# Kernel tuning notes

Hardware: AMD Instinct MI355X
Metric: run time of the kernel (lower is better)

The kernel has to match this reference:

```python
import jax, jax.numpy as jnp
import numpy as np

N, E, C = 4096, 32768, 64
IN, H, HEADS, L = 128, 256, 4, 2
HD = H // HEADS


def setup_inputs() -> dict:
    key = jax.random.key(0)
    ks = iter(jax.random.split(key, 40))
    s = lambda *sh: jax.random.normal(next(ks), sh, jnp.float32) * 0.05
    inp = {
        "node_features": jax.random.normal(next(ks), (N, IN), jnp.float32),
        "edges": jax.random.randint(next(ks), (E, 2), 0, N),
        "candidates": jax.random.randint(next(ks), (C, 2), 0, N),
        # GRUCell(input_dim, hidden_dim): torch layout w_ih [3H, IN], w_hh [3H, H]
        "gru_w_ih": s(3 * H, IN), "gru_w_hh": s(3 * H, H),
        "gru_b_ih": s(3 * H), "gru_b_hh": s(3 * H),
        # GraphTransformer: L layers of MHA + LN + FFN, stacked over layer dim
        "attn_in_w": s(L, 3 * H, H), "attn_in_b": s(L, 3 * H),
        "attn_out_w": s(L, H, H), "attn_out_b": s(L, H),
        "ln1_g": jnp.ones((L, H), jnp.float32), "ln1_b": jnp.zeros((L, H), jnp.float32),
        "ffn_w1": s(L, 4 * H, H), "ffn_b1": s(L, 4 * H),
        "ffn_w2": s(L, H, 4 * H), "ffn_b2": s(L, H),
        "ln2_g": jnp.ones((L, H), jnp.float32), "ln2_b": jnp.zeros((L, H), jnp.float32),
        # SCN
        "scn_w1": s(H, H), "scn_b1": s(H), "scn_w2": s(H, H), "scn_b2": s(H),
        # EdgePredictor: Linear(2H, H) -> ReLU -> Linear(H, 1)
        "ep_w1": s(H, 2 * H), "ep_b1": s(H), "ep_w2": s(1, H), "ep_b2": s(1),
    }
    return inp


def _layernorm(x, g, b, eps=1e-5):
    m = jnp.mean(x, -1, keepdims=True)
    v = jnp.mean((x - m) ** 2, -1, keepdims=True)
    return g * (x - m) / jnp.sqrt(v + eps) + b


def _mha(x, in_w, in_b, out_w, out_b):
    # x: [N, H]; torch MultiheadAttention self-attention, batch=1
    qkv = x @ in_w.T + in_b                      # [N, 3H]
    q, k, v = jnp.split(qkv, 3, axis=-1)
    q = q.reshape(N, HEADS, HD).transpose(1, 0, 2)  # [heads, N, hd]
    k = k.reshape(N, HEADS, HD).transpose(1, 0, 2)
    v = v.reshape(N, HEADS, HD).transpose(1, 0, 2)
    scores = jnp.einsum('hqd,hkd->hqk', q, k) / jnp.sqrt(jnp.float32(HD))
    a = jax.nn.softmax(scores, axis=-1)
    o = jnp.einsum('hqk,hkd->hqd', a, v).transpose(1, 0, 2).reshape(N, H)
    return o @ out_w.T + out_b


def _run_memory(node_features, edges, gru_w_ih, gru_w_hh, gru_b_ih, gru_b_hh):
    # input-gate contribution depends only on src feature: vectorize upfront
    gi_all = node_features[edges[:, 0]] @ gru_w_ih.T + gru_b_ih  # [E, 3H]

    def step(mem, inp):
        gi, dst = inp
        h = mem[dst]                                   # gather [H]
        gh = h @ gru_w_hh.T + gru_b_hh                 # [3H]
        ir, iz, inn = jnp.split(gi, 3)
        hr, hz, hn = jnp.split(gh, 3)
        r = jax.nn.sigmoid(ir + hr)
        z = jax.nn.sigmoid(iz + hz)
        n = jnp.tanh(inn + r * hn)
        h_new = (1.0 - z) * n + z * h                  # torch GRUCell update
        return mem.at[dst].set(h_new), None

    mem0 = jnp.zeros((N, H), jnp.float32)
    mem, _ = jax.lax.scan(step, mem0, (gi_all, edges[:, 1]))
    return mem


def reference(node_features, edges, candidates, gru_w_ih, gru_w_hh, gru_b_ih, gru_b_hh,
              attn_in_w, attn_in_b, attn_out_w, attn_out_b, ln1_g, ln1_b,
              ffn_w1, ffn_b1, ffn_w2, ffn_b2, ln2_g, ln2_b,
              scn_w1, scn_b1, scn_w2, scn_b2, ep_w1, ep_b1, ep_w2, ep_b2):
    mem = _run_memory(node_features, edges, gru_w_ih, gru_w_hh, gru_b_ih, gru_b_hh)
    x = jax.lax.stop_gradient(mem)   # original writes memory with .detach()
    for l in range(L):
        a = _mha(x, attn_in_w[l], attn_in_b[l], attn_out_w[l], attn_out_b[l])
        x = _layernorm(x + a, ln1_g[l], ln1_b[l])
        f = jax.nn.relu(x @ ffn_w1[l].T + ffn_b1[l]) @ ffn_w2[l].T + ffn_b2[l]
        x = _layernorm(x + f, ln2_g[l], ln2_b[l])
    refined = jax.nn.relu(x @ scn_w1.T + scn_b1) @ scn_w2.T + scn_b2
    h = jnp.concatenate([refined[candidates[:, 0]], refined[candidates[:, 1]]], axis=-1)  # [C, 2H]
    logits = jax.nn.relu(h @ ep_w1.T + ep_b1) @ ep_w2.T + ep_b2  # [C, 1]
    return jax.nn.sigmoid(logits).squeeze(-1)
```

## Files before the change

### kernel.cpp

```cpp
#include <hip/hip_runtime.h>
#include <math.h>

#define NN     4096
#define NE     32768
#define NCAND  64
#define IND    128
#define HDM    256
#define NL     2
#define MAXD   64
#define GNPB   16
#define NS     4

typedef __attribute__((ext_vector_type(8))) short short8;
typedef __attribute__((ext_vector_type(4))) float f32x4;

__device__ __forceinline__ float sigf(float x) { return 1.0f / (1.0f + __expf(-x)); }
__device__ __forceinline__ float tanh_fast(float x) {
  float e = __expf(-2.0f * fabsf(x));
  float r = (1.0f - e) / (1.0f + e);
  return x < 0.0f ? -r : r;
}
__device__ __forceinline__ unsigned short f2bf(float f) {
  unsigned int x = __float_as_uint(f);
  x += 0x7fffu + ((x >> 16) & 1u);
  return (unsigned short)(x >> 16);
}
__device__ __forceinline__ float bf2f(unsigned short u) {
  return __uint_as_float(((unsigned int)u) << 16);
}

#define CVT_TOT 2523136
__global__ __launch_bounds__(256) void cvt_weights(
    const float* __restrict__ nf, const float* __restrict__ wih,
    const float* __restrict__ ain, const float* __restrict__ aout,
    const float* __restrict__ f1, const float* __restrict__ f2,
    const float* __restrict__ s1, const float* __restrict__ s2,
    const float* __restrict__ whh, unsigned short* __restrict__ dst) {
  const size_t e = ((size_t)blockIdx.x * 256 + threadIdx.x) * 4;
  if (e >= CVT_TOT) return;
  const float* src;
  if (e < 524288)       src = nf   + e;
  else if (e < 622592)  src = wih  + (e - 524288);
  else if (e < 1015808) src = ain  + (e - 622592);
  else if (e < 1146880) src = aout + (e - 1015808);
  else if (e < 1671168) src = f1   + (e - 1146880);
  else if (e < 2195456) src = f2   + (e - 1671168);
  else if (e < 2260992) src = s1   + (e - 2195456);
  else if (e < 2326528) src = s2   + (e - 2260992);
  else                  src = whh  + (e - 2326528);
  const float4 v = *(const float4*)src;
  dst[e + 0] = f2bf(v.x); dst[e + 1] = f2bf(v.y);
  dst[e + 2] = f2bf(v.z); dst[e + 3] = f2bf(v.w);
}

__global__ __launch_bounds__(256) void build_pos(const int* __restrict__ edges,
                                                 int* __restrict__ cnt, int* __restrict__ lists) {
  const int e = blockIdx.x * 256 + threadIdx.x;
  const int d = edges[2 * e + 1];
  const int slot = atomicAdd(&cnt[d], 1);
  if (slot < MAXD) lists[(size_t)d * MAXD + slot] = e;
}

__global__ __launch_bounds__(256) void sort_srcs(const int* __restrict__ edges,
                                                 int* __restrict__ cnt,
                                                 const int* __restrict__ lists,
                                                 int* __restrict__ srcs,
                                                 int* __restrict__ hist) {
  __shared__ int Ls[256][65];
  const int t = threadIdx.x;
  const int d = blockIdx.x * 256 + t;
  int c = cnt[d]; if (c > MAXD) c = MAXD;
  for (int i = 0; i < c; ++i) Ls[t][i] = lists[(size_t)d * MAXD + i];
  for (int i = 1; i < c; ++i) {
    const int key = Ls[t][i];
    int j = i - 1;
    while (j >= 0 && Ls[t][j] > key) { Ls[t][j + 1] = Ls[t][j]; --j; }
    Ls[t][j + 1] = key;
  }
  for (int i = 0; i < c; ++i) srcs[(size_t)d * MAXD + i] = edges[2 * Ls[t][i]];
  cnt[d] = c;
  atomicAdd(&hist[c], 1);
}

__global__ void scan_prep(const int* __restrict__ hist, int* __restrict__ cursor) {
  const int t = threadIdx.x;
  if (t <= MAXD) {
    int ss = 0;
    for (int dd = t + 1; dd <= MAXD; ++dd) ss += hist[dd];
    cursor[t] = ss;
  }
}

__global__ __launch_bounds__(256) void perm_scatter(const int* __restrict__ cnt,
                                                    int* __restrict__ cursor, int* __restrict__ perm) {
  const int d = blockIdx.x * 256 + threadIdx.x;
  const int rank = atomicAdd(&cursor[cnt[d]], 1);
  perm[rank] = d;
}

__global__ void prep_bias(const float* __restrict__ b_ih, const float* __restrict__ b_hh,
                          float* __restrict__ bias_gx) {
  const int t = blockIdx.x * 256 + threadIdx.x;
  if (t < 768) bias_gx[t] = b_ih[t] + (t < 512 ? b_hh[t] : 0.0f);
}

template <int ACT, int GS, int OMODE>
__global__ __launch_bounds__(256) void gemm_bf16(
    const unsigned short* __restrict__ A, const int* __restrict__ gidx,
    const unsigned short* __restrict__ W, const float* __restrict__ bias,
    float* __restrict__ C, unsigned short* __restrict__ Cb,
    int M, int N, int K) {
  __shared__ unsigned short As[64 * 64];
  __shared__ unsigned short Ws[64 * 64];
  __shared__ int ridx[64];
  const int bm = blockIdx.y * 64, bn = blockIdx.x * 64;
  const int tid = threadIdx.x;
  const int ln = tid & 63, w = tid >> 6;
  const int jc = ln & 15, kq = ln >> 4;
  const int srow = tid >> 2, q = tid & 3;

  if constexpr (GS > 0) {
    if (tid < 64) ridx[tid] = gidx[(size_t)(bm + tid) * GS];
    __syncthreads();
  }
  const size_t arow = (GS > 0) ? (size_t)ridx[srow] : (size_t)(bm + srow);
  const unsigned short* Asrc = A + arow * K + q * 16;
  const unsigned short* Wsrc = W + (size_t)(bn + srow) * K + q * 16;

  f32x4 acc[2][2];
#pragma unroll
  for (int i = 0; i < 2; ++i)
#pragma unroll
    for (int j = 0; j < 2; ++j) acc[i][j] = (f32x4){0.f, 0.f, 0.f, 0.f};
  const int mrow = (w >> 1) * 32, ncol = (w & 1) * 32;
  const int sb0 = (q * 32) ^ ((srow & 7) << 4);
  const int sb1 = (q * 32 + 16) ^ ((srow & 7) << 4);

  for (int k0 = 0; k0 < K; k0 += 64) {
    __syncthreads();
    {
      const short8 a0 = *(const short8*)(Asrc + k0);
      const short8 a1 = *(const short8*)(Asrc + k0 + 8);
      const short8 w0 = *(const short8*)(Wsrc + k0);
      const short8 w1 = *(const short8*)(Wsrc + k0 + 8);
      *(short8*)((char*)As + srow * 128 + sb0) = a0;
      *(short8*)((char*)As + srow * 128 + sb1) = a1;
      *(short8*)((char*)Ws + srow * 128 + sb0) = w0;
      *(short8*)((char*)Ws + srow * 128 + sb1) = w1;
    }
    __syncthreads();
#pragma unroll
    for (int kt = 0; kt < 2; ++kt) {
      const int kb = kt * 64 + kq * 16;
      short8 a[2], bb[2];
#pragma unroll
      for (int i = 0; i < 2; ++i) {
        const int ra = mrow + i * 16 + jc;
        a[i] = *(const short8*)((const char*)As + ra * 128 + (kb ^ ((ra & 7) << 4)));
        const int rb = ncol + i * 16 + jc;
        bb[i] = *(const short8*)((const char*)Ws + rb * 128 + (kb ^ ((rb & 7) << 4)));
      }
#pragma unroll
      for (int mi = 0; mi < 2; ++mi)
#pragma unroll
        for (int ni = 0; ni < 2; ++ni)
          acc[mi][ni] = __builtin_amdgcn_mfma_f32_16x16x32_bf16(a[mi], bb[ni], acc[mi][ni], 0, 0, 0);
    }
  }
#pragma unroll
  for (int mi = 0; mi < 2; ++mi)
#pragma unroll
    for (int ni = 0; ni < 2; ++ni) {
      const int col = bn + ncol + ni * 16 + jc;
      const float bs = bias[col];
#pragma unroll
      for (int v = 0; v < 4; ++v) {
        const int row = bm + mrow + mi * 16 + kq * 4 + v;
        float val = acc[mi][ni][v] + bs;
        if (ACT == 1) val = fmaxf(val, 0.0f);
        if constexpr (OMODE != 2) C[(size_t)row * N + col] = val;
        if constexpr (OMODE >= 1) Cb[(size_t)row * N + col] = f2bf(val);
      }
    }
}

__global__ __launch_bounds__(512, 1) void gru_reg(
    const int* __restrict__ perm, const int* __restrict__ cnt,
    const int* __restrict__ srcs, const unsigned short* __restrict__ gx,
    const unsigned short* __restrict__ whhb, const float* __restrict__ b_hh,
    float* __restrict__ x, unsigned short* __restrict__ xb) {
  const int tid = threadIdx.x;
  const int w = tid >> 6;
  const int ln = tid & 63;
  const int jc = ln & 15, kq = ln >> 4;
  const int grow = tid >> 5, gpart = tid & 31;

  __shared__ unsigned short Ah[GNPB * 256];
  __shared__ unsigned short Gi[GNPB * 776];
  __shared__ int srcs_s[GNPB][MAXD];
  __shared__ int node_s[GNPB], cnt_s[GNPB];
  __shared__ int Rb_s;

  if (tid < GNPB) {
    const int node = perm[blockIdx.x * GNPB + tid];
    node_s[tid] = node;
    cnt_s[tid] = cnt[node];
  }
  for (int i = tid; i < GNPB * 256; i += 512) Ah[i] = 0;
  __syncthreads();
  for (int i = tid; i < GNPB * MAXD; i += 512)
    srcs_s[i >> 6][i & 63] = srcs[(size_t)node_s[i >> 6] * MAXD + (i & 63)];
  if (tid == 0) {
    int mx = 0;
    for (int i = 0; i < GNPB; ++i) mx = mx > cnt_s[i] ? mx : cnt_s[i];
    Rb_s = mx;
  }

  short8 W[48];
#pragma unroll
  for (int g = 0; g < 3; ++g)
#pragma unroll
    for (int ct = 0; ct < 2; ++ct) {
      const unsigned short* src =
          whhb + (size_t)(g * 256 + w * 32 + ct * 16 + jc) * 256 + kq * 8;
#pragma unroll
      for (int kt = 0; kt < 8; ++kt)
        W[(g * 2 + ct) * 8 + kt] = *(const short8*)(src + kt * 32);
    }
  float bhN[2];
  bhN[0] = b_hh[512 + w * 32 + jc];
  bhN[1] = b_hh[512 + w * 32 + 16 + jc];

  float h[8];
#pragma unroll
  for (int i = 0; i < 8; ++i) h[i] = 0.f;

  __syncthreads();
  const int Rb = Rb_s;
  const int myc = cnt_s[grow];

  for (int r = 0; r < Rb; ++r) {
    const int sn = (r < myc) ? srcs_s[grow][r] : 0;
    const unsigned short* gsrc = gx + (size_t)sn * 768 + gpart * 24;
    const short8 gv0 = *(const short8*)gsrc;
    const short8 gv1 = *(const short8*)(gsrc + 8);
    const short8 gv2 = *(const short8*)(gsrc + 16);

    f32x4 acc[6];
#pragma unroll
    for (int i = 0; i < 6; ++i) acc[i] = (f32x4){0.f, 0.f, 0.f, 0.f};
#pragma unroll
    for (int kt = 0; kt < 8; ++kt) {
      const short8 a = *(const short8*)((const char*)Ah + jc * 512 +
                                        ((kt * 64 + kq * 16) ^ ((jc & 7) << 4)));
#pragma unroll
      for (int t = 0; t < 6; ++t)
        acc[t] = __builtin_amdgcn_mfma_f32_16x16x32_bf16(a, W[t * 8 + kt], acc[t], 0, 0, 0);
    }
    {
      unsigned short* gdst = Gi + grow * 776 + gpart * 24;
      *(short8*)gdst = gv0;
      *(short8*)(gdst + 8) = gv1;
      *(short8*)(gdst + 16) = gv2;
    }
    __syncthreads();
#pragma unroll
    for (int ct = 0; ct < 2; ++ct) {
      const int col = w * 32 + ct * 16 + jc;
#pragma unroll
      for (int v = 0; v < 4; ++v) {
        const int nd = kq * 4 + v;
        if (r < cnt_s[nd]) {
          const float giR = bf2f(Gi[nd * 776 + col]);
          const float giZ = bf2f(Gi[nd * 776 + 256 + col]);
          const float giN = bf2f(Gi[nd * 776 + 512 + col]);
          const float rr = sigf(giR + acc[ct][v]);
          const float zz = sigf(giZ + acc[2 + ct][v]);
          const float nn2 = tanh_fast(giN + rr * (acc[4 + ct][v] + bhN[ct]));
          const float hn = (1.0f - zz) * nn2 + zz * h[ct * 4 + v];
          h[ct * 4 + v] = hn;
          *(unsigned short*)((char*)Ah + nd * 512 + ((col * 2) ^ ((nd & 7) << 4))) = f2bf(hn);
        }
      }
    }
    __syncthreads();
  }
#pragma unroll
  for (int ct = 0; ct < 2; ++ct) {
    const int col = w * 32 + ct * 16 + jc;
#pragma unroll
    for (int v = 0; v < 4; ++v) {
      const int gnode = node_s[kq * 4 + v];
      x[(size_t)gnode * HDM + col] = h[ct * 4 + v];
      xb[(size_t)gnode * HDM + col] = f2bf(h[ct * 4 + v]);
    }
  }
}

__global__ __launch_bounds__(256) void transpose_v(const unsigned short* __restrict__ qkvb,
                                                   unsigned short* __restrict__ vtb) {
  const int h = blockIdx.y, nt = blockIdx.x;
  __shared__ unsigned short T[64][72];
  const int t = threadIdx.x;
  const int r = t >> 2, c = (t & 3) << 4;
  {
    const unsigned short* src = qkvb + (size_t)(nt * 64 + r) * 768 + 512 + h * 64 + c;
    *(short8*)&T[r][c] = *(const short8*)src;
    *(short8*)&T[r][c + 8] = *(const short8*)(src + 8);
  }
  __syncthreads();
  {
    short8 o0, o1;
#pragma unroll
    for (int j = 0; j < 8; ++j) { o0[j] = (short)T[c + j][r]; o1[j] = (short)T[c + 8 + j][r]; }
    unsigned short* dst = vtb + (size_t)(h * 64 + r) * 4096 + nt * 64 + c;
    *(short8*)dst = o0;
    *(short8*)(dst + 8) = o1;
  }
}

__global__ __launch_bounds__(256) void flash_part(
    const unsigned short* __restrict__ qkvb, const unsigned short* __restrict__ vtb,
    float* __restrict__ Op, float* __restrict__ lp) {
  const int h = blockIdx.y;
  const int qb = blockIdx.x * 64;
  const int z = blockIdx.z;
  const int tid = threadIdx.x;
  const int ln = tid & 63, w = tid >> 6;
  const int jc = ln & 15, kq = ln >> 4;
  __shared__ unsigned short Ks[2][64 * 64];
  __shared__ unsigned short Vts[2][64 * 64];
  __shared__ unsigned short Ps[4][16 * 64];

  short8 aq[2];
  {
    const unsigned short* qsrc = qkvb + (size_t)(qb + w * 16 + jc) * 768 + h * 64 + kq * 8;
    aq[0] = *(const short8*)qsrc;
    aq[1] = *(const short8*)(qsrc + 32);
  }
  f32x4 accO[4];
#pragma unroll
  for (int nf = 0; nf < 4; ++nf) accO[nf] = (f32x4){0.f, 0.f, 0.f, 0.f};
  float psum[4] = {0.f, 0.f, 0.f, 0.f};

  const int srow = tid >> 2, sc = tid & 3;
  const int swb0 = (sc * 32) ^ ((srow & 7) << 4);
  const int swb1 = (sc * 32 + 16) ^ ((srow & 7) << 4);
  const int k0 = z * 1024;
  unsigned short* Pw = Ps[w];

  short8 kr0, kr1, vr0, vr1;
  {
    const unsigned short* ksrc = qkvb + (size_t)(k0 + srow) * 768 + 256 + h * 64 + sc * 16;
    kr0 = *(const short8*)ksrc; kr1 = *(const short8*)(ksrc + 8);
    const unsigned short* vsrc = vtb + (size_t)(h * 64 + srow) * 4096 + k0 + sc * 16;
    vr0 = *(const short8*)vsrc; vr1 = *(const short8*)(vsrc + 8);
  }

  for (int t = 0; t < 16; ++t) {
    const int cur = t & 1;
    *(short8*)((char*)Ks[cur] + srow * 128 + swb0) = kr0;
    *(short8*)((char*)Ks[cur] + srow * 128 + swb1) = kr1;
    *(short8*)((char*)Vts[cur] + srow * 128 + swb0) = vr0;
    *(short8*)((char*)Vts[cur] + srow * 128 + swb1) = vr1;
    {
      const int tn = t < 15 ? t + 1 : 15;
      const unsigned short* ksrc =
          qkvb + (size_t)(k0 + tn * 64 + srow) * 768 + 256 + h * 64 + sc * 16;
      kr0 = *(const short8*)ksrc; kr1 = *(const short8*)(ksrc + 8);
      const unsigned short* vsrc =
          vtb + (size_t)(h * 64 + srow) * 4096 + k0 + tn * 64 + sc * 16;
      vr0 = *(const short8*)vsrc; vr1 = *(const short8*)(vsrc + 8);
    }
    __syncthreads();
    f32x4 s[4];
#pragma unroll
    for (int kt = 0; kt < 4; ++kt) s[kt] = (f32x4){0.f, 0.f, 0.f, 0.f};
    __builtin_amdgcn_s_setprio(1);
#pragma unroll
    for (int ks = 0; ks < 2; ++ks) {
#pragma unroll
      for (int kt = 0; kt < 4; ++kt) {
        const int brow = kt * 16 + jc;
        const short8 bk = *(const short8*)((const char*)Ks[cur] + brow * 128 +
                                           ((ks * 64 + kq * 16) ^ ((brow & 7) << 4)));
        s[kt] = __builtin_amdgcn_mfma_f32_16x16x32_bf16(aq[ks], bk, s[kt], 0, 0, 0);
      }
    }
    __builtin_amdgcn_s_setprio(0);
#pragma unroll
    for (int kt = 0; kt < 4; ++kt) {
#pragma unroll
      for (int v = 0; v < 4; ++v) {
        const float pv = __expf(s[kt][v] * 0.125f - 8.0f);
        psum[v] += pv;
        const int pr = kq * 4 + v;
        const int cb = kt * 32 + jc * 2;
        *(unsigned short*)((char*)Pw + pr * 128 + (cb ^ ((pr & 7) << 4))) = f2bf(pv);
      }
    }
    asm volatile("s_waitcnt lgkmcnt(0)" ::: "memory");
    __builtin_amdgcn_sched_barrier(0);
    __builtin_amdgcn_s_setprio(1);
#pragma unroll
    for (int ks = 0; ks < 2; ++ks) {
      const short8 ap = *(const short8*)((const char*)Pw + jc * 128 +
                                         ((ks * 64 + kq * 16) ^ ((jc & 7) << 4)));
#pragma unroll
      for (int nf = 0; nf < 4; ++nf) {
        const int brow = nf * 16 + jc;
        const short8 bv = *(const short8*)((const char*)Vts[cur] + brow * 128 +
                                           ((ks * 64 + kq * 16) ^ ((brow & 7) << 4)));
        accO[nf] = __builtin_amdgcn_mfma_f32_16x16x32_bf16(ap, bv, accO[nf], 0, 0, 0);
      }
    }
    __builtin_amdgcn_s_setprio(0);
  }
#pragma unroll
  for (int v = 0; v < 4; ++v) {
    float ps = psum[v];
    ps += __shfl_xor(ps, 1);
    ps += __shfl_xor(ps, 2);
    ps += __shfl_xor(ps, 4);
    ps += __shfl_xor(ps, 8);
    psum[v] = ps;
  }
  float* opb = Op + ((size_t)z * NN + qb + w * 16 + kq * 4) * HDM + h * 64 + jc;
#pragma unroll
  for (int nf = 0; nf < 4; ++nf)
#pragma unroll
    for (int v = 0; v < 4; ++v)
      opb[(size_t)v * HDM + nf * 16] = accO[nf][v];
  if (jc == 0) {
#pragma unroll
    for (int v = 0; v < 4; ++v)
      lp[((size_t)z * 4 + h) * NN + qb + w * 16 + kq * 4 + v] = psum[v];
  }
}

__global__ __launch_bounds__(256) void attn_combine(const float* __restrict__ Op,
                                                    const float* __restrict__ lp,
                                                    unsigned short* __restrict__ outb) {
  const int row = blockIdx.x * 4 + (threadIdx.x >> 6);
  const int lane = threadIdx.x & 63;
  const int col = lane * 4;
  const int h = col >> 6;
  float l = 0.f;
  float4 o = {0.f, 0.f, 0.f, 0.f};
#pragma unroll
  for (int z = 0; z < NS; ++z) {
    l += lp[((size_t)z * 4 + h) * NN + row];
    const float4 p = *(const float4*)(Op + ((size_t)z * NN + row) * HDM + col);
    o.x += p.x; o.y += p.y; o.z += p.z; o.w += p.w;
  }
  const float inv = 1.0f / l;
  unsigned short* d = outb + (size_t)row * HDM + col;
  d[0] = f2bf(o.x * inv); d[1] = f2bf(o.y * inv);
  d[2] = f2bf(o.z * inv); d[3] = f2bf(o.w * inv);
}

__global__ __launch_bounds__(256) void ln_residual(float* __restrict__ x,
                                                   const float* __restrict__ a,
                                                   const float* __restrict__ g,
                                                   const float* __restrict__ b,
                                                   unsigned short* __restrict__ xb) {
  const int lane = threadIdx.x & 63;
  const int row = blockIdx.x * 4 + (threadIdx.x >> 6);
  float v[4];
  float s = 0.0f;
#pragma unroll
  for (int j = 0; j < 4; j++) {
    const int col = j * 64 + lane;
    v[j] = x[(size_t)row * HDM + col] + a[(size_t)row * HDM + col];
    s += v[j];
  }
#pragma unroll
  for (int off = 32; off > 0; off >>= 1) s += __shfl_xor(s, off);
  const float mu = s * (1.0f / HDM);
  float vs = 0.0f;
#pragma unroll
  for (int j = 0; j < 4; j++) {
    const float d = v[j] - mu;
    vs += d * d;
  }
#pragma unroll
  for (int off = 32; off > 0; off >>= 1) vs += __shfl_xor(vs, off);
  const float rinv = 1.0f / sqrtf(vs * (1.0f / HDM) + 1e-5f);
#pragma unroll
  for (int j = 0; j < 4; j++) {
    const int col = j * 64 + lane;
    const float val = g[col] * (v[j] - mu) * rinv + b[col];
    x[(size_t)row * HDM + col] = val;
    xb[(size_t)row * HDM + col] = f2bf(val);
  }
}

template <int ACT>
__global__ __launch_bounds__(256) void gemm_bias(const float* __restrict__ A,
                                                 const float* __restrict__ W,
                                                 const float* __restrict__ bias,
                                                 float* __restrict__ C, int M, int NCo, int K) {
  __shared__ float As[16][65];
  __shared__ float Ws[16][65];
  const int bm = blockIdx.y * 64, bn = blockIdx.x * 64;
  const int tid = threadIdx.x;
  const int tx = tid & 15, ty = tid >> 4;
  const int lr = tid >> 2;
  const int lk = (tid & 3) * 4;
  float acc[4][4] = {{0.0f}};
  for (int k0 = 0; k0 < K; k0 += 16) {
    __syncthreads();
    {
      const float4 a4 = *(const float4*)(A + (size_t)(bm + lr) * K + k0 + lk);
      As[lk + 0][lr] = a4.x; As[lk + 1][lr] = a4.y; As[lk + 2][lr] = a4.z; As[lk + 3][lr] = a4.w;
      const float4 w4 = *(const float4*)(W + (size_t)(bn + lr) * K + k0 + lk);
      Ws[lk + 0][lr] = w4.x; Ws[lk + 1][lr] = w4.y; Ws[lk + 2][lr] = w4.z; Ws[lk + 3][lr] = w4.w;
    }
    __syncthreads();
#pragma unroll
    for (int k = 0; k < 16; k++) {
      const float a0 = As[k][ty * 4 + 0], a1 = As[k][ty * 4 + 1];
      const float a2 = As[k][ty * 4 + 2], a3 = As[k][ty * 4 + 3];
      const float w0 = Ws[k][tx * 4 + 0], w1 = Ws[k][tx * 4 + 1];
      const float w2 = Ws[k][tx * 4 + 2], w3 = Ws[k][tx * 4 + 3];
      acc[0][0] += a0 * w0; acc[0][1] += a0 * w1; acc[0][2] += a0 * w2; acc[0][3] += a0 * w3;
      acc[1][0] += a1 * w0; acc[1][1] += a1 * w1; acc[1][2] += a1 * w2; acc[1][3] += a1 * w3;
      acc[2][0] += a2 * w0; acc[2][1] += a2 * w1; acc[2][2] += a2 * w2; acc[2][3] += a2 * w3;
      acc[3][0] += a3 * w0; acc[3][1] += a3 * w1; acc[3][2] += a3 * w2; acc[3][3] += a3 * w3;
    }
  }
  const float b0 = bias[bn + tx * 4 + 0], b1 = bias[bn + tx * 4 + 1];
  const float b2 = bias[bn + tx * 4 + 2], b3 = bias[bn + tx * 4 + 3];
#pragma unroll
  for (int i = 0; i < 4; i++) {
    float4 o;
    o.x = acc[i][0] + b0; o.y = acc[i][1] + b1; o.z = acc[i][2] + b2; o.w = acc[i][3] + b3;
    if (ACT == 1) {
      o.x = fmaxf(o.x, 0.0f); o.y = fmaxf(o.y, 0.0f);
      o.z = fmaxf(o.z, 0.0f); o.w = fmaxf(o.w, 0.0f);
    }
    *(float4*)(C + (size_t)(bm + ty * 4 + i) * NCo + bn + tx * 4) = o;
  }
}

__global__ void gather_cat(const float* __restrict__ refined, const int* __restrict__ cand,
                           float* __restrict__ hcat) {
  const int c = blockIdx.x;
  const int t = threadIdx.x;
  const int n0 = cand[2 * c], n1 = cand[2 * c + 1];
  hcat[(size_t)c * 512 + t] = (t < 256) ? refined[(size_t)n0 * HDM + t]
                                        : refined[(size_t)n1 * HDM + (t - 256)];
}

__global__ void ep_final(const float* __restrict__ eph, const float* __restrict__ w2,
                         const float* __restrict__ b2, float* __restrict__ out) {
  const int c = blockIdx.x;
  const int lane = threadIdx.x;
  float s = 0.0f;
#pragma unroll
  for (int j = 0; j < 4; j++) s += eph[(size_t)c * HDM + j * 64 + lane] * w2[j * 64 + lane];
#pragma unroll
  for (int off = 32; off > 0; off >>= 1) s += __shfl_xor(s, off);
  if (lane == 0) out[c] = 1.0f / (1.0f + __expf(-(s + b2[0])));
}

extern "C" void kernel_launch(void* const* d_in, const int* in_sizes, int n_in,
                              void* d_out, int out_size, void* d_ws, size_t ws_size,
                              hipStream_t stream) {
  (void)in_sizes; (void)n_in; (void)out_size; (void)ws_size;
  const float* nf    = (const float*)d_in[0];
  const int*   edges = (const int*)d_in[1];
  const int*   cand  = (const int*)d_in[2];
  const float* w_ih  = (const float*)d_in[3];
  const float* w_hh  = (const float*)d_in[4];
  const float* b_ih  = (const float*)d_in[5];
  const float* b_hh  = (const float*)d_in[6];
  const float* ain_w = (const float*)d_in[7];
  const float* ain_b = (const float*)d_in[8];
  const float* aout_w = (const float*)d_in[9];
  const float* aout_b = (const float*)d_in[10];
  const float* ln1g = (const float*)d_in[11];
  const float* ln1b = (const float*)d_in[12];
  const float* f1w  = (const float*)d_in[13];
  const float* f1b  = (const float*)d_in[14];
  const float* f2w  = (const float*)d_in[15];
  const float* f2b  = (const float*)d_in[16];
  const float* ln2g = (const float*)d_in[17];
  const float* ln2b = (const float*)d_in[18];
  const float* s1w  = (const float*)d_in[19];
  const float* s1b  = (const float*)d_in[20];
  const float* s2w  = (const float*)d_in[21];
  const float* s2b  = (const float*)d_in[22];
  const float* e1w  = (const float*)d_in[23];
  const float* e1b  = (const float*)d_in[24];
  const float* e2w  = (const float*)d_in[25];
  const float* e2b  = (const float*)d_in[26];
  float* out = (float*)d_out;

  char* wp = (char*)d_ws;
  float* x        = (float*)wp; wp += (size_t)NN * HDM * 4;
  unsigned short* xb = (unsigned short*)wp; wp += (size_t)NN * HDM * 2;
  unsigned short* wseg = (unsigned short*)wp; wp += (size_t)CVT_TOT * 2;
  int* cnt        = (int*)wp;  wp += (size_t)NN * 4;
  int* lists      = (int*)wp;  wp += (size_t)NN * MAXD * 4;
  int* srcs       = (int*)wp;  wp += (size_t)NN * MAXD * 4;
  int* meta       = (int*)wp;  wp += 256 * 4;
  float* bias_gx  = (float*)wp; wp += 1024 * 4;
  int* perm       = (int*)wp;  wp += (size_t)NN * 4;
  unsigned short* gx = (unsigned short*)wp; wp += (size_t)NN * 768 * 2;
  char* uni       = wp;
  unsigned short* qkvb   = (unsigned short*)uni;
  unsigned short* vtb    = (unsigned short*)(uni + 6291456);
  float* abuf    = (float*)(uni + 8388608);
  unsigned short* abuf_b = (unsigned short*)(uni + 12582912);
  float* fbuf    = (float*)(uni + 14680064);
  float* Op      = fbuf;
  unsigned short* fbuf_b = (unsigned short*)(uni + 31457280);
  float* lp      = (float*)(uni + 31457280);
  float* refined = (float*)(uni + 39845888);
  float* hcat    = (float*)(uni + 44040192);
  float* eph     = (float*)(uni + 44171264);

  unsigned short* nf_b  = wseg;
  unsigned short* wihb  = wseg + 524288;
  unsigned short* ainb  = wseg + 622592;
  unsigned short* aoutb = wseg + 1015808;
  unsigned short* f1b_  = wseg + 1146880;
  unsigned short* f2b_  = wseg + 1671168;
  unsigned short* s1b_  = wseg + 2195456;
  unsigned short* s2b_  = wseg + 2260992;
  unsigned short* whhb  = wseg + 2326528;

  int* hist   = meta;
  int* cursor = meta + 128;

  hipMemsetAsync(cnt, 0, (size_t)NN * 4, stream);
  hipMemsetAsync(meta, 0, 256 * 4, stream);

  cvt_weights<<<2464, 256, 0, stream>>>(nf, w_ih, ain_w, aout_w, f1w, f2w, s1w, s2w, w_hh, wseg);
  build_pos<<<NE / 256, 256, 0, stream>>>(edges, cnt, lists);
  sort_srcs<<<NN / 256, 256, 0, stream>>>(edges, cnt, lists, srcs, hist);
  scan_prep<<<1, 128, 0, stream>>>(hist, cursor);
  perm_scatter<<<NN / 256, 256, 0, stream>>>(cnt, cursor, perm);
  prep_bias<<<3, 256, 0, stream>>>(b_ih, b_hh, bias_gx);

  gemm_bf16<0, 0, 2><<<dim3(12, NN / 64), 256, 0, stream>>>(
      nf_b, nullptr, wihb, bias_gx, nullptr, gx, NN, 768, IND);
  gru_reg<<<NN / GNPB, 512, 0, stream>>>(perm, cnt, srcs, gx, whhb, b_hh, x, xb);

  for (int l = 0; l < NL; l++) {
    gemm_bf16<0, 0, 2><<<dim3(12, 64), 256, 0, stream>>>(
        xb, nullptr, ainb + (size_t)l * 196608, ain_b + l * 768, nullptr, qkvb, NN, 768, HDM);
    transpose_v<<<dim3(64, 4), 256, 0, stream>>>(qkvb, vtb);
    flash_part<<<dim3(64, 4, NS), 256, 0, stream>>>(qkvb, vtb, Op, lp);
    attn_combine<<<NN / 4, 256, 0, stream>>>(Op, lp, abuf_b);
    gemm_bf16<0, 0, 0><<<dim3(4, 64), 256, 0, stream>>>(
        abuf_b, nullptr, aoutb + (size_t)l * 65536, aout_b + l * 256, fbuf, nullptr, NN, 256, HDM);
    ln_residual<<<NN / 4, 256, 0, stream>>>(x, fbuf, ln1g + l * 256, ln1b + l * 256, xb);
    gemm_bf16<1, 0, 2><<<dim3(16, 64), 256, 0, stream>>>(
        xb, nullptr, f1b_ + (size_t)l * 262144, f1b + l * 1024, nullptr, fbuf_b, NN, 1024, HDM);
    gemm_bf16<0, 0, 0><<<dim3(4, 64), 256, 0, stream>>>(
        fbuf_b, nullptr, f2b_ + (size_t)l * 262144, f2b + l * 256, abuf, nullptr, NN, 256, 1024);
    ln_residual<<<NN / 4, 256, 0, stream>>>(x, abuf, ln2g + l * 256, ln2b + l * 256, xb);
  }

  gemm_bf16<1, 0, 1><<<dim3(4, 64), 256, 0, stream>>>(
      xb, nullptr, s1b_, s1b, abuf, abuf_b, NN, 256, HDM);
  gemm_bf16<0, 0, 0><<<dim3(4, 64), 256, 0, stream>>>(
      abuf_b, nullptr, s2b_, s2b, refined, nullptr, NN, 256, HDM);
  gather_cat<<<NCAND, 512, 0, stream>>>(refined, cand, hcat);
  gemm_bias<1><<<dim3(4, 1), 256, 0, stream>>>(hcat, e1w, e1b, eph, NCAND, 256, 512);
  ep_final<<<NCAND, 64, 0, stream>>>(eph, e2w, e2b, out);
}
```

Baseline: 390.9 us.

## Fuse small kernels, write transposed V in QKV GEMM, prefetch GRU inputs

Merges the bias prep into the scan kernel and folds gather, edge-predictor GEMM and final sigmoid into one ep_fused kernel, cutting launch count. The QKV GEMM epilogue now also writes V transposed directly, so the separate transpose_v pass and its round trip through memory go away. The GRU recurrence loop software-prefetches the next step's gate inputs from global memory before the MFMA work to hide load latency. The transposed-V stores are narrow and strided, and the fused edge predictor reads fp32 weights per thread without tiling.

```diff
diff --git a/kernel.cpp b/kernel.cpp
--- a/kernel.cpp
+++ b/kernel.cpp
@@ -12,6 +12,7 @@
 #define NS     4
 
 typedef __attribute__((ext_vector_type(8))) short short8;
+typedef __attribute__((ext_vector_type(4))) short short4b;
 typedef __attribute__((ext_vector_type(4))) float f32x4;
 
 __device__ __forceinline__ float sigf(float x) { return 1.0f / (1.0f + __expf(-x)); }
@@ -82,12 +83,21 @@
   atomicAdd(&hist[c], 1);
 }
 
-__global__ void scan_prep(const int* __restrict__ hist, int* __restrict__ cursor) {
-  const int t = threadIdx.x;
-  if (t <= MAXD) {
-    int ss = 0;
-    for (int dd = t + 1; dd <= MAXD; ++dd) ss += hist[dd];
-    cursor[t] = ss;
+__global__ __launch_bounds__(256) void scan_prep(const int* __restrict__ hist,
+                                                 int* __restrict__ cursor,
+                                                 const float* __restrict__ b_ih,
+                                                 const float* __restrict__ b_hh,
+                                                 float* __restrict__ bias_gx) {
+  if (blockIdx.x == 3) {
+    const int t = threadIdx.x;
+    if (t <= MAXD) {
+      int ss = 0;
+      for (int dd = t + 1; dd <= MAXD; ++dd) ss += hist[dd];
+      cursor[t] = ss;
+    }
+  } else {
+    const int gt = blockIdx.x * 256 + threadIdx.x;
+    if (gt < 768) bias_gx[gt] = b_ih[gt] + (gt < 512 ? b_hh[gt] : 0.0f);
   }
 }
 
@@ -98,18 +108,12 @@
   perm[rank] = d;
 }
 
-__global__ void prep_bias(const float* __restrict__ b_ih, const float* __restrict__ b_hh,
-                          float* __restrict__ bias_gx) {
-  const int t = blockIdx.x * 256 + threadIdx.x;
-  if (t < 768) bias_gx[t] = b_ih[t] + (t < 512 ? b_hh[t] : 0.0f);
-}
-
-template <int ACT, int GS, int OMODE>
+template <int ACT, int GS, int OMODE, int VT>
 __global__ __launch_bounds__(256) void gemm_bf16(
     const unsigned short* __restrict__ A, const int* __restrict__ gidx,
     const unsigned short* __restrict__ W, const float* __restrict__ bias,
     float* __restrict__ C, unsigned short* __restrict__ Cb,
-    int M, int N, int K) {
+    unsigned short* __restrict__ Vt, int M, int N, int K) {
   __shared__ unsigned short As[64 * 64];
   __shared__ unsigned short Ws[64 * 64];
   __shared__ int ridx[64];
@@ -173,13 +177,26 @@
     for (int ni = 0; ni < 2; ++ni) {
       const int col = bn + ncol + ni * 16 + jc;
       const float bs = bias[col];
+      float vals[4];
+#pragma unroll
+      for (int v = 0; v < 4; ++v) {
+        float val = acc[mi][ni][v] + bs;
+        if (ACT == 1) val = fmaxf(val, 0.0f);
+        vals[v] = val;
+      }
 #pragma unroll
       for (int v = 0; v < 4; ++v) {
         const int row = bm + mrow + mi * 16 + kq * 4 + v;
-        float val = acc[mi][ni][v] + bs;
-        if (ACT == 1) val = fmaxf(val, 0.0f);
-        if constexpr (OMODE != 2) C[(size_t)row * N + col] = val;
-        if constexpr (OMODE >= 1) Cb[(size_t)row * N + col] = f2bf(val);
+        if constexpr (OMODE != 2) C[(size_t)row * N + col] = vals[v];
+        if constexpr (OMODE >= 1) Cb[(size_t)row * N + col] = f2bf(vals[v]);
+      }
+      if constexpr (VT == 1) {
+        if (bn >= 512) {
+          short4b p;
+#pragma unroll
+          for (int v = 0; v < 4; ++v) p[v] = (short)f2bf(vals[v]);
+          *(short4b*)(Vt + (size_t)(col - 512) * NN + bm + mrow + mi * 16 + kq * 4) = p;
+        }
       }
     }
 }
@@ -239,29 +256,36 @@
   const int Rb = Rb_s;
   const int myc = cnt_s[grow];
 
+  short8 gv0, gv1, gv2;
+  {
+    const int sn = (0 < myc) ? srcs_s[grow][0] : 0;
+    const unsigned short* gs = gx + (size_t)sn * 768 + gpart * 24;
+    gv0 = *(const short8*)gs; gv1 = *(const short8*)(gs + 8); gv2 = *(const short8*)(gs + 16);
+  }
+
   for (int r = 0; r < Rb; ++r) {
-    const int sn = (r < myc) ? srcs_s[grow][r] : 0;
-    const unsigned short* gsrc = gx + (size_t)sn * 768 + gpart * 24;
-    const short8 gv0 = *(const short8*)gsrc;
-    const short8 gv1 = *(const short8*)(gsrc + 8);
-    const short8 gv2 = *(const short8*)(gsrc + 16);
-
-    f32x4 acc[6];
-#pragma unroll
-    for (int i = 0; i < 6; ++i) acc[i] = (f32x4){0.f, 0.f, 0.f, 0.f};
-#pragma unroll
-    for (int kt = 0; kt < 8; ++kt) {
-      const short8 a = *(const short8*)((const char*)Ah + jc * 512 +
-                                        ((kt * 64 + kq * 16) ^ ((jc & 7) << 4)));
-#pragma unroll
-      for (int t = 0; t < 6; ++t)
-        acc[t] = __builtin_amdgcn_mfma_f32_16x16x32_bf16(a, W[t * 8 + kt], acc[t], 0, 0, 0);
-    }
     {
       unsigned short* gdst = Gi + grow * 776 + gpart * 24;
       *(short8*)gdst = gv0;
       *(short8*)(gdst + 8) = gv1;
       *(short8*)(gdst + 16) = gv2;
+    }
+    {
+      const int rn = r + 1;
+      const int sn = (rn < myc) ? srcs_s[grow][rn] : 0;
+      const unsigned short* gs = gx + (size_t)sn * 768 + gpart * 24;
+      gv0 = *(const short8*)gs; gv1 = *(const short8*)(gs + 8); gv2 = *(const short8*)(gs + 16);
+    }
+    f32x4 acc[6];
+#pragma unroll
+    for (int i = 0; i < 6; ++i) acc[i] = (f32x4){0.f, 0.f, 0.f, 0.f};
+#pragma unroll
+    for (int kt = 0; kt < 8; ++kt) {
+      const short8 a = *(const short8*)((const char*)Ah + jc * 512 +
+                                        ((kt * 64 + kq * 16) ^ ((jc & 7) << 4)));
+#pragma unroll
+      for (int t = 0; t < 6; ++t)
+        acc[t] = __builtin_amdgcn_mfma_f32_16x16x32_bf16(a, W[t * 8 + kt], acc[t], 0, 0, 0);
     }
     __syncthreads();
 #pragma unroll
@@ -294,28 +318,6 @@
       x[(size_t)gnode * HDM + col] = h[ct * 4 + v];
       xb[(size_t)gnode * HDM + col] = f2bf(h[ct * 4 + v]);
     }
-  }
-}
-
-__global__ __launch_bounds__(256) void transpose_v(const unsigned short* __restrict__ qkvb,
-                                                   unsigned short* __restrict__ vtb) {
-  const int h = blockIdx.y, nt = blockIdx.x;
-  __shared__ unsigned short T[64][72];
-  const int t = threadIdx.x;
-  const int r = t >> 2, c = (t & 3) << 4;
-  {
-    const unsigned short* src = qkvb + (size_t)(nt * 64 + r) * 768 + 512 + h * 64 + c;
-    *(short8*)&T[r][c] = *(const short8*)src;
-    *(short8*)&T[r][c + 8] = *(const short8*)(src + 8);
-  }
-  __syncthreads();
-  {
-    short8 o0, o1;
-#pragma unroll
-    for (int j = 0; j < 8; ++j) { o0[j] = (short)T[c + j][r]; o1[j] = (short)T[c + 8 + j][r]; }
-    unsigned short* dst = vtb + (size_t)(h * 64 + r) * 4096 + nt * 64 + c;
-    *(short8*)dst = o0;
-    *(short8*)(dst + 8) = o1;
   }
 }
 
@@ -495,73 +497,39 @@
   }
 }
 
-template <int ACT>
-__global__ __launch_bounds__(256) void gemm_bias(const float* __restrict__ A,
-                                                 const float* __restrict__ W,
-                                                 const float* __restrict__ bias,
-                                                 float* __restrict__ C, int M, int NCo, int K) {
-  __shared__ float As[16][65];
-  __shared__ float Ws[16][65];
-  const int bm = blockIdx.y * 64, bn = blockIdx.x * 64;
-  const int tid = threadIdx.x;
-  const int tx = tid & 15, ty = tid >> 4;
-  const int lr = tid >> 2;
-  const int lk = (tid & 3) * 4;
-  float acc[4][4] = {{0.0f}};
-  for (int k0 = 0; k0 < K; k0 += 16) {
-    __syncthreads();
-    {
-      const float4 a4 = *(const float4*)(A + (size_t)(bm + lr) * K + k0 + lk);
-      As[lk + 0][lr] = a4.x; As[lk + 1][lr] = a4.y; As[lk + 2][lr] = a4.z; As[lk + 3][lr] = a4.w;
-      const float4 w4 = *(const float4*)(W + (size_t)(bn + lr) * K + k0 + lk);
-      Ws[lk + 0][lr] = w4.x; Ws[lk + 1][lr] = w4.y; Ws[lk + 2][lr] = w4.z; Ws[lk + 3][lr] = w4.w;
-    }
-    __syncthreads();
-#pragma unroll
-    for (int k = 0; k < 16; k++) {
-      const float a0 = As[k][ty * 4 + 0], a1 = As[k][ty * 4 + 1];
-      const float a2 = As[k][ty * 4 + 2], a3 = As[k][ty * 4 + 3];
-      const float w0 = Ws[k][tx * 4 + 0], w1 = Ws[k][tx * 4 + 1];
-      const float w2 = Ws[k][tx * 4 + 2], w3 = Ws[k][tx * 4 + 3];
-      acc[0][0] += a0 * w0; acc[0][1] += a0 * w1; acc[0][2] += a0 * w2; acc[0][3] += a0 * w3;
-      acc[1][0] += a1 * w0; acc[1][1] += a1 * w1; acc[1][2] += a1 * w2; acc[1][3] += a1 * w3;
-      acc[2][0] += a2 * w0; acc[2][1] += a2 * w1; acc[2][2] += a2 * w2; acc[2][3] += a2 * w3;
-      acc[3][0] += a3 * w0; acc[3][1] += a3 * w1; acc[3][2] += a3 * w2; acc[3][3] += a3 * w3;
-    }
-  }
-  const float b0 = bias[bn + tx * 4 + 0], b1 = bias[bn + tx * 4 + 1];
-  const float b2 = bias[bn + tx * 4 + 2], b3 = bias[bn + tx * 4 + 3];
-#pragma unroll
-  for (int i = 0; i < 4; i++) {
-    float4 o;
-    o.x = acc[i][0] + b0; o.y = acc[i][1] + b1; o.z = acc[i][2] + b2; o.w = acc[i][3] + b3;
-    if (ACT == 1) {
-      o.x = fmaxf(o.x, 0.0f); o.y = fmaxf(o.y, 0.0f);
-      o.z = fmaxf(o.z, 0.0f); o.w = fmaxf(o.w, 0.0f);
-    }
-    *(float4*)(C + (size_t)(bm + ty * 4 + i) * NCo + bn + tx * 4) = o;
-  }
-}
-
-__global__ void gather_cat(const float* __restrict__ refined, const int* __restrict__ cand,
-                           float* __restrict__ hcat) {
+__global__ __launch_bounds__(256) void ep_fused(const float* __restrict__ refined,
+                                                const int* __restrict__ cand,
+                                                const float* __restrict__ e1w,
+                                                const float* __restrict__ e1b,
+                                                const float* __restrict__ e2w,
+                                                const float* __restrict__ e2b,
+                                                float* __restrict__ out) {
   const int c = blockIdx.x;
   const int t = threadIdx.x;
+  __shared__ float hrow[512];
+  __shared__ float eph_s[256];
   const int n0 = cand[2 * c], n1 = cand[2 * c + 1];
-  hcat[(size_t)c * 512 + t] = (t < 256) ? refined[(size_t)n0 * HDM + t]
-                                        : refined[(size_t)n1 * HDM + (t - 256)];
-}
-
-__global__ void ep_final(const float* __restrict__ eph, const float* __restrict__ w2,
-                         const float* __restrict__ b2, float* __restrict__ out) {
-  const int c = blockIdx.x;
-  const int lane = threadIdx.x;
-  float s = 0.0f;
-#pragma unroll
-  for (int j = 0; j < 4; j++) s += eph[(size_t)c * HDM + j * 64 + lane] * w2[j * 64 + lane];
-#pragma unroll
-  for (int off = 32; off > 0; off >>= 1) s += __shfl_xor(s, off);
-  if (lane == 0) out[c] = 1.0f / (1.0f + __expf(-(s + b2[0])));
+  hrow[t] = refined[(size_t)n0 * HDM + t];
+  hrow[256 + t] = refined[(size_t)n1 * HDM + t];
+  __syncthreads();
+  const float4* wrow = (const float4*)(e1w + (size_t)t * 512);
+  float s = 0.f;
+#pragma unroll 8
+  for (int k = 0; k < 128; ++k) {
+    const float4 w4 = wrow[k];
+    const float4 h4 = *(const float4*)(hrow + k * 4);
+    s += w4.x * h4.x + w4.y * h4.y + w4.z * h4.z + w4.w * h4.w;
+  }
+  eph_s[t] = fmaxf(s + e1b[t], 0.0f);
+  __syncthreads();
+  if (t < 64) {
+    float p = 0.f;
+#pragma unroll
+    for (int j = 0; j < 4; ++j) p += eph_s[j * 64 + t] * e2w[j * 64 + t];
+#pragma unroll
+    for (int off = 32; off > 0; off >>= 1) p += __shfl_xor(p, off);
+    if (t == 0) out[c] = 1.0f / (1.0f + __expf(-(p + e2b[0])));
+  }
 }
 
 extern "C" void kernel_launch(void* const* d_in, const int* in_sizes, int n_in,
@@ -618,8 +586,6 @@
   unsigned short* fbuf_b = (unsigned short*)(uni + 31457280);
   float* lp      = (float*)(uni + 31457280);
   float* refined = (float*)(uni + 39845888);
-  float* hcat    = (float*)(uni + 44040192);
-  float* eph     = (float*)(uni + 44171264);
 
   unsigned short* nf_b  = wseg;
   unsigned short* wihb  = wseg + 524288;
@@ -640,35 +606,31 @@
   cvt_weights<<<2464, 256, 0, stream>>>(nf, w_ih, ain_w, aout_w, f1w, f2w, s1w, s2w, w_hh, wseg);
   build_pos<<<NE / 256, 256, 0, stream>>>(edges, cnt, lists);
   sort_srcs<<<NN / 256, 256, 0, stream>>>(edges, cnt, lists, srcs, hist);
-  scan_prep<<<1, 128, 0, stream>>>(hist, cursor);
+  scan_prep<<<4, 256, 0, stream>>>(hist, cursor, b_ih, b_hh, bias_gx);
   perm_scatter<<<NN / 256, 256, 0, stream>>>(cnt, cursor, perm);
-  prep_bias<<<3, 256, 0, stream>>>(b_ih, b_hh, bias_gx);
-
-  gemm_bf16<0, 0, 2><<<dim3(12, NN / 64), 256, 0, stream>>>(
-      nf_b, nullptr, wihb, bias_gx, nullptr, gx, NN, 768, IND);
+
+  gemm_bf16<0, 0, 2, 0><<<dim3(12, NN / 64), 256, 0, stream>>>(
+      nf_b, nullptr, wihb, bias_gx, nullptr, gx, nullptr, NN, 768, IND);
   gru_reg<<<NN / GNPB, 512, 0, stream>>>(perm, cnt, srcs, gx, whhb, b_hh, x, xb);
 
   for (int l = 0; l < NL; l++) {
-    gemm_bf16<0, 0, 2><<<dim3(12, 64), 256, 0, stream>>>(
-        xb, nullptr, ainb + (size_t)l * 196608, ain_b + l * 768, nullptr, qkvb, NN, 768, HDM);
-    transpose_v<<<dim3(64, 4), 256, 0, stream>>>(qkvb, vtb);
+    gemm_bf16<0, 0, 2, 1><<<dim3(12, 64), 256, 0, stream>>>(
+        xb, nullptr, ainb + (size_t)l * 196608, ain_b + l * 768, nullptr, qkvb, vtb, NN, 768, HDM);
     flash_part<<<dim3(64, 4, NS), 256, 0, stream>>>(qkvb, vtb, Op, lp);
     attn_combine<<<NN / 4, 256, 0, stream>>>(Op, lp, abuf_b);
-    gemm_bf16<0, 0, 0><<<dim3(4, 64), 256, 0, stream>>>(
-        abuf_b, nullptr, aoutb + (size_t)l * 65536, aout_b + l * 256, fbuf, nullptr, NN, 256, HDM);
+    gemm_bf16<0, 0, 0, 0><<<dim3(4, 64), 256, 0, stream>>>(
+        abuf_b, nullptr, aoutb + (size_t)l * 65536, aout_b + l * 256, fbuf, nullptr, nullptr, NN, 256, HDM);
     ln_residual<<<NN / 4, 256, 0, stream>>>(x, fbuf, ln1g + l * 256, ln1b + l * 256, xb);
-    gemm_bf16<1, 0, 2><<<dim3(16, 64), 256, 0, stream>>>(
-        xb, nullptr, f1b_ + (size_t)l * 262144, f1b + l * 1024, nullptr, fbuf_b, NN, 1024, HDM);
-    gemm_bf16<0, 0, 0><<<dim3(4, 64), 256, 0, stream>>>(
-        fbuf_b, nullptr, f2b_ + (size_t)l * 262144, f2b + l * 256, abuf, nullptr, NN, 256, 1024);
+    gemm_bf16<1, 0, 2, 0><<<dim3(16, 64), 256, 0, stream>>>(
+        xb, nullptr, f1b_ + (size_t)l * 262144, f1b + l * 1024, nullptr, fbuf_b, nullptr, NN, 1024, HDM);
+    gemm_bf16<0, 0, 0, 0><<<dim3(4, 64), 256, 0, stream>>>(
+        fbuf_b, nullptr, f2b_ + (size_t)l * 262144, f2b + l * 256, abuf, nullptr, nullptr, NN, 256, 1024);
     ln_residual<<<NN / 4, 256, 0, stream>>>(x, abuf, ln2g + l * 256, ln2b + l * 256, xb);
   }
 
-  gemm_bf16<1, 0, 1><<<dim3(4, 64), 256, 0, stream>>>(
-      xb, nullptr, s1b_, s1b, abuf, abuf_b, NN, 256, HDM);
-  gemm_bf16<0, 0, 0><<<dim3(4, 64), 256, 0, stream>>>(
-      abuf_b, nullptr, s2b_, s2b, refined, nullptr, NN, 256, HDM);
-  gather_cat<<<NCAND, 512, 0, stream>>>(refined, cand, hcat);
-  gemm_bias<1><<<dim3(4, 1), 256, 0, stream>>>(hcat, e1w, e1b, eph, NCAND, 256, 512);
-  ep_final<<<NCAND, 64, 0, stream>>>(eph, e2w, e2b, out);
-}
+  gemm_bf16<1, 0, 1, 0><<<dim3(4, 64), 256, 0, stream>>>(
+      xb, nullptr, s1b_, s1b, abuf, abuf_b, nullptr, NN, 256, HDM);
+  gemm_bf16<0, 0, 0, 0><<<dim3(4, 64), 256, 0, stream>>>(
+      abuf_b, nullptr, s2b_, s2b, refined, nullptr, nullptr, NN, 256, HDM);
+  ep_fused<<<NCAND, 256, 0, stream>>>(refined, cand, e1w, e1b, e2w, e2b, out);
+}
```

After: 358.6 us. 1.09x faster.
